# Kernel tuning notes

Measured on AMD Instinct MI355X. Metric: run time of the kernel, lower is better.

The kernel has to match this reference:

```python
import jax, jax.numpy as jnp
import numpy as np

B, S, IN_DIM, P_DIM, H = 2, 2048, 1024, 512, 8
HD = P_DIM // H
N_PENTA = 1024
SCALES = (128, 256, 512)
K_NEIGH = max(16, min(int(S * 0.15), 128))  # adaptive window -> 128
SCALE = 1.0 / float(np.sqrt(HD))
EPS = 1e-5


def _ln(x, g, b):
    mu = jnp.mean(x, axis=-1, keepdims=True)
    var = jnp.mean((x - mu) ** 2, axis=-1, keepdims=True)
    return (x - mu) * jax.lax.rsqrt(var + EPS) * g + b


def setup_inputs() -> dict:
    key = jax.random.key(0)
    ks = list(jax.random.split(key, 6 + 2 * len(SCALES)))
    w = lambda k, shp: jax.random.normal(k, shp, jnp.float32) * 0.02
    inp = {
        'sequence_features': jax.random.normal(ks[0], (B, S, IN_DIM), jnp.float32),
        'shared_pentachora': jax.random.normal(ks[1], (N_PENTA, 5, P_DIM), jnp.float32),
        'shared_positions': jax.random.uniform(ks[2], (N_PENTA,), dtype=jnp.float32),
        'proj_W': w(ks[3], (IN_DIM, P_DIM)), 'proj_b': jnp.zeros((P_DIM,), jnp.float32),
        'ln_g': jnp.ones((P_DIM,), jnp.float32), 'ln_b': jnp.zeros((P_DIM,), jnp.float32),
        'qkv_W': w(ks[4], (P_DIM, 3 * P_DIM)), 'qkv_b': jnp.zeros((3 * P_DIM,), jnp.float32),
        'out_W': w(ks[5], (P_DIM, P_DIM)), 'out_b': jnp.zeros((P_DIM,), jnp.float32),
    }
    i = 6
    for s in SCALES:
        inp[f'w1_{s}'] = w(ks[i], (P_DIM, 2 * s)); inp[f'b1_{s}'] = jnp.zeros((2 * s,), jnp.float32)
        inp[f'g_{s}'] = jnp.ones((2 * s,), jnp.float32); inp[f'bb_{s}'] = jnp.zeros((2 * s,), jnp.float32)
        inp[f'w2_{s}'] = w(ks[i + 1], (2 * s, s)); inp[f'b2_{s}'] = jnp.zeros((s,), jnp.float32)
        i += 2
    return inp


def _attend_one(z_b, pos_b, qkv_W, qkv_b, out_W, out_b):
    # z_b: [S, P_DIM], pos_b: [S]
    qkv = (z_b @ qkv_W + qkv_b).reshape(S, 3, H, HD)
    q = jnp.transpose(qkv[:, 0], (1, 0, 2))  # [H, S, HD]
    k = jnp.transpose(qkv[:, 1], (1, 0, 2))
    v = jnp.transpose(qkv[:, 2], (1, 0, 2))
    dist = jnp.abs(pos_b[:, None] - pos_b[None, :])  # [S, S]
    _, routes = jax.lax.top_k(-dist, K_NEIGH)        # [S, K] nearest in Cantor space
    kg = k[:, routes, :]  # [H, S, K, HD] gathered keys
    vg = v[:, routes, :]
    scores = jnp.einsum('hqd,hqkd->hqk', q, kg) * SCALE
    attn = jax.nn.softmax(scores, axis=-1)
    out = jnp.einsum('hqk,hqkd->hqd', attn, vg)
    out = jnp.transpose(out, (1, 0, 2)).reshape(S, P_DIM)
    return out @ out_W + out_b


def reference(sequence_features, shared_pentachora, shared_positions, proj_W, proj_b, ln_g, ln_b, qkv_W, qkv_b, out_W, out_b, w1_128, b1_128, g_128, bb_128, w2_128, b2_128, w1_256, b1_256, g_256, bb_256, w2_256, b2_256, w1_512, b1_512, g_512, bb_512, w2_512, b2_512):
    # centroids from pentachora vertices, L2-normalized
    cent = shared_pentachora.mean(axis=1)
    cent = cent / jnp.clip(jnp.linalg.norm(cent, axis=-1, keepdims=True), 1e-12)
    # input projection -> LN -> GELU -> L2 normalize
    z = jax.nn.gelu(_ln(sequence_features @ proj_W + proj_b, ln_g, ln_b), approximate=False)
    z = z / jnp.clip(jnp.linalg.norm(z, axis=-1, keepdims=True), 1e-12)
    # match to opinion anchors, inherit Cantor positions
    anchor_ids = jnp.argmax(jnp.einsum('bnd,pd->bnp', z, cent), axis=-1)  # [B, S]
    cantor_positions = shared_positions[anchor_ids]  # [B, S]
    # per-sample geometric sparse attention (vmapped over batch)
    z_att = jax.vmap(_attend_one, in_axes=(0, 0, None, None, None, None))(
        z, cantor_positions, qkv_W, qkv_b, out_W, out_b)  # [B, S, P_DIM]
    pooled = z_att.mean(axis=1)  # [B, P_DIM] (no attention mask)
    scale_params = (
        (w1_128, b1_128, g_128, bb_128, w2_128, b2_128),
        (w1_256, b1_256, g_256, bb_256, w2_256, b2_256),
        (w1_512, b1_512, g_512, bb_512, w2_512, b2_512),
    )
    outs = []
    for (w1, b1, g, bb, w2, b2) in scale_params:
        h = jax.nn.gelu(_ln(pooled @ w1 + b1, g, bb), approximate=False)
        outs.append(h @ w2 + b2)
    return jnp.concatenate(outs, axis=-1)  # [B, 128+256+512] concatenated scale opinions
```

## Files before the change

kernel.cpp:

```cpp
#include <hip/hip_runtime.h>
#include <math.h>

#define DEV __device__ __forceinline__

static constexpr int S_LEN  = 2048;
static constexpr int IN_DIM = 1024;
static constexpr int P_DIM  = 512;
static constexpr int NHEAD  = 8;
static constexpr int HD     = 64;
static constexpr int KN     = 128;

typedef __attribute__((ext_vector_type(8))) short bf16x8;
typedef __attribute__((ext_vector_type(4))) float f32x4;

DEV float gelu_exact(float x) {
    return 0.5f * x * (1.0f + erff(x * 0.70710678118654752440f));
}

DEV short bf_hi(float x) {
    unsigned u = __float_as_uint(x);
    unsigned r = (u + 0x7fffu + ((u >> 16) & 1u)) >> 16;
    return (short)r;
}
DEV float bf_f(short h) { return __uint_as_float(((unsigned)(unsigned short)h) << 16); }

DEV float block_reduce_sum(float v, float* sm4) {
    #pragma unroll
    for (int off = 32; off; off >>= 1) v += __shfl_down(v, off, 64);
    int lane = threadIdx.x & 63, w = threadIdx.x >> 6;
    __syncthreads();
    if (lane == 0) sm4[w] = v;
    __syncthreads();
    return sm4[0] + sm4[1] + sm4[2] + sm4[3];
}

DEV void wt_body(const float* __restrict__ W, short* __restrict__ WTh,
                 short* __restrict__ WTl, int K, int N, int bk, int bn,
                 float (*tile)[65]) {
    int t = threadIdx.x;
    int c = t & 63, r4 = t >> 6;
    #pragma unroll
    for (int i = 0; i < 16; i++) {
        int row = r4 + i * 4;
        tile[row][c] = W[(long)(bk * 64 + row) * N + bn * 64 + c];
    }
    __syncthreads();
    #pragma unroll
    for (int i = 0; i < 16; i++) {
        int n = r4 + i * 4;
        float v = tile[c][n];
        short h = bf_hi(v);
        long o = (long)(bn * 64 + n) * K + bk * 64 + c;
        WTh[o] = h;
        WTl[o] = bf_hi(v - bf_f(h));
    }
}

__global__ __launch_bounds__(256) void k_prep(const float* __restrict__ penta,
                                              short* __restrict__ ch, short* __restrict__ cl,
                                              const float* __restrict__ projW,
                                              short* __restrict__ pjh, short* __restrict__ pjl,
                                              const float* __restrict__ qkvW,
                                              short* __restrict__ qkh, short* __restrict__ qkl,
                                              const float* __restrict__ seq,
                                              short* __restrict__ sh, short* __restrict__ sl,
                                              unsigned long long* __restrict__ rowkey,
                                              float* __restrict__ pooledZ) {
    __shared__ float tile[64][65];
    __shared__ float sm4[4];
    int blk = blockIdx.x, t = threadIdx.x;
    if (blk < 1024) {
        int p = blk;
        if (t < 4) rowkey[p * 4 + t] = 0ull;
        if (p < 4) pooledZ[p * 256 + t] = 0.f;
        float c0 = 0.f, c1 = 0.f;
        #pragma unroll
        for (int v = 0; v < 5; v++) {
            const float* row = penta + ((long)p * 5 + v) * P_DIM;
            c0 += row[t];
            c1 += row[t + 256];
        }
        c0 /= 5.0f; c1 /= 5.0f;
        float tot = block_reduce_sum(c0 * c0 + c1 * c1, sm4);
        float n = fmaxf(sqrtf(tot), 1e-12f);
        float v0 = c0 / n, v1 = c1 / n;
        short h0 = bf_hi(v0), h1 = bf_hi(v1);
        ch[p * P_DIM + t]       = h0;
        ch[p * P_DIM + t + 256] = h1;
        cl[p * P_DIM + t]       = bf_hi(v0 - bf_f(h0));
        cl[p * P_DIM + t + 256] = bf_hi(v1 - bf_f(h1));
    } else if (blk < 1152) {
        int id = blk - 1024;
        wt_body(projW, pjh, pjl, IN_DIM, P_DIM, id & 15, id >> 4, tile);
    } else if (blk < 1344) {
        int id = blk - 1152;
        wt_body(qkvW, qkh, qkl, P_DIM, 3 * P_DIM, id & 7, id >> 3, tile);
    } else {
        long base = ((long)(blk - 1344) * 256 + t) * 16;
        #pragma unroll
        for (int u = 0; u < 4; u++) {
            float4 v = *(const float4*)(seq + base + u * 4);
            short h0 = bf_hi(v.x), h1 = bf_hi(v.y), h2 = bf_hi(v.z), h3 = bf_hi(v.w);
            *(short4*)(sh + base + u * 4) = make_short4(h0, h1, h2, h3);
            *(short4*)(sl + base + u * 4) =
                make_short4(bf_hi(v.x - bf_f(h0)), bf_hi(v.y - bf_f(h1)),
                            bf_hi(v.z - bf_f(h2)), bf_hi(v.w - bf_f(h3)));
        }
    }
}

template <int BM, int K, int N, int EPI>
__global__ __launch_bounds__(256) void k_mm(const short* __restrict__ Ash,
                                            const short* __restrict__ Asl,
                                            const short* __restrict__ BTh,
                                            const short* __restrict__ BTl,
                                            const float* __restrict__ bias,
                                            float* __restrict__ C,
                                            unsigned long long* __restrict__ rowkey) {
    constexpr int TI  = BM / 32;
    constexpr int CA  = BM / 8;
    constexpr int NCH = 2 * CA + 32;
    __shared__ __align__(128) short AhS[BM * 64], AlS[BM * 64];
    __shared__ __align__(128) short BhS[128 * 64], BlS[128 * 64];
    int t = threadIdx.x;
    int lane = t & 63, wave = t >> 6;
    int wr = (wave >> 1) * (BM / 2), wc = (wave & 1) * 64;
    int m = lane & 15, quad = lane >> 4;
    int rb = blockIdx.x * BM, cb = blockIdx.y * 128;
    int r8 = lane >> 3, p8 = lane & 7;
    int sl = p8 ^ r8;

    f32x4 acc[TI][4];
    #pragma unroll
    for (int i = 0; i < TI; i++)
        #pragma unroll
        for (int j = 0; j < 4; j++) acc[i][j] = (f32x4){0.f, 0.f, 0.f, 0.f};

    for (int k0 = 0; k0 < K; k0 += 64) {
        __syncthreads();
        for (int c = wave; c < NCH; c += 4) {
            const short* src; short* dst;
            if (c < CA) {
                src = Ash + (long)(rb + c * 8 + r8) * K + k0 + sl * 8;
                dst = AhS + c * 512;
            } else if (c < 2 * CA) {
                int cc = c - CA;
                src = Asl + (long)(rb + cc * 8 + r8) * K + k0 + sl * 8;
                dst = AlS + cc * 512;
            } else if (c < 2 * CA + 16) {
                int cc = c - 2 * CA;
                src = BTh + (long)(cb + cc * 8 + r8) * K + k0 + sl * 8;
                dst = BhS + cc * 512;
            } else {
                int cc = c - 2 * CA - 16;
                src = BTl + (long)(cb + cc * 8 + r8) * K + k0 + sl * 8;
                dst = BlS + cc * 512;
            }
            __builtin_amdgcn_global_load_lds(
                (const __attribute__((address_space(1))) unsigned int*)src,
                (__attribute__((address_space(3))) unsigned int*)dst, 16, 0, 0);
        }
        __syncthreads();

        #pragma unroll
        for (int ks = 0; ks < 2; ks++) {
            int so = ((ks * 4 + quad) ^ (m & 7)) * 8;
            bf16x8 ah[TI], al[TI], bh[4], bl[4];
            #pragma unroll
            for (int i = 0; i < TI; i++) {
                int off = (wr + i * 16 + m) * 64 + so;
                ah[i] = *(const bf16x8*)(AhS + off);
                al[i] = *(const bf16x8*)(AlS + off);
            }
            #pragma unroll
            for (int j = 0; j < 4; j++) {
                int off = (wc + j * 16 + m) * 64 + so;
                bh[j] = *(const bf16x8*)(BhS + off);
                bl[j] = *(const bf16x8*)(BlS + off);
            }
            #pragma unroll
            for (int i = 0; i < TI; i++)
                #pragma unroll
                for (int j = 0; j < 4; j++) {
                    acc[i][j] = __builtin_amdgcn_mfma_f32_16x16x32_bf16(ah[i], bh[j], acc[i][j], 0, 0, 0);
                    acc[i][j] = __builtin_amdgcn_mfma_f32_16x16x32_bf16(ah[i], bl[j], acc[i][j], 0, 0, 0);
                    acc[i][j] = __builtin_amdgcn_mfma_f32_16x16x32_bf16(al[i], bh[j], acc[i][j], 0, 0, 0);
                }
        }
    }

    if (EPI == 0) {
        #pragma unroll
        for (int i = 0; i < TI; i++) {
            int gr0 = rb + wr + i * 16 + quad * 4;
            #pragma unroll
            for (int j = 0; j < 4; j++) {
                int gc = cb + wc + j * 16 + m;
                float bv = bias[gc];
                #pragma unroll
                for (int r = 0; r < 4; r++)
                    C[(long)(gr0 + r) * N + gc] = acc[i][j][r] + bv;
            }
        }
    } else {
        #pragma unroll
        for (int i = 0; i < TI; i++) {
            #pragma unroll
            for (int r = 0; r < 4; r++) {
                int gr = rb + wr + i * 16 + quad * 4 + r;
                float bv = acc[i][0][r];
                int bp = cb + wc + m;
                #pragma unroll
                for (int j = 1; j < 4; j++) {
                    float v = acc[i][j][r];
                    int p = cb + wc + j * 16 + m;
                    if (v > bv) { bv = v; bp = p; }
                }
                #pragma unroll
                for (int off = 1; off < 16; off <<= 1) {
                    float ov = __shfl_xor(bv, off, 64);
                    int op = __shfl_xor(bp, off, 64);
                    if (ov > bv || (ov == bv && op < bp)) { bv = ov; bp = op; }
                }
                if (m == 0) {
                    unsigned u = __float_as_uint(bv);
                    u = (u & 0x80000000u) ? ~u : (u | 0x80000000u);
                    unsigned long long key =
                        ((unsigned long long)u << 32) | (unsigned)(0xFFFFFFFFu - (unsigned)bp);
                    atomicMax(&rowkey[gr], key);
                }
            }
        }
    }
}

__global__ __launch_bounds__(256) void k_ln_gelu_norm(const float* __restrict__ Zin,
                                                      const float* __restrict__ g,
                                                      const float* __restrict__ b,
                                                      short* __restrict__ z_h,
                                                      short* __restrict__ z_l) {
    long row = blockIdx.x;
    int t = threadIdx.x;
    __shared__ float sm4[4];
    float x0 = Zin[row * P_DIM + t], x1 = Zin[row * P_DIM + t + 256];
    float mu = block_reduce_sum(x0 + x1, sm4) * (1.0f / P_DIM);
    float d0 = x0 - mu, d1 = x1 - mu;
    float var = block_reduce_sum(d0 * d0 + d1 * d1, sm4) * (1.0f / P_DIM);
    float rs = 1.0f / sqrtf(var + 1e-5f);
    float y0 = gelu_exact(d0 * rs * g[t] + b[t]);
    float y1 = gelu_exact(d1 * rs * g[t + 256] + b[t + 256]);
    float nn = block_reduce_sum(y0 * y0 + y1 * y1, sm4);
    float n = fmaxf(sqrtf(nn), 1e-12f);
    float v0 = y0 / n, v1 = y1 / n;
    short h0 = bf_hi(v0), h1 = bf_hi(v1);
    z_h[row * P_DIM + t]       = h0;
    z_h[row * P_DIM + t + 256] = h1;
    z_l[row * P_DIM + t]       = bf_hi(v0 - bf_f(h0));
    z_l[row * P_DIM + t + 256] = bf_hi(v1 - bf_f(h1));
}

__global__ __launch_bounds__(256) void k_rank(const unsigned long long* __restrict__ rowkey,
                                              const float* __restrict__ spos,
                                              int* __restrict__ order,
                                              float* __restrict__ pos_srt) {
    int b = blockIdx.y, t = threadIdx.x;
    __shared__ unsigned long long key[2048];
    for (int u = 0; u < 8; u++) {
        int i = t + u * 256;
        unsigned p = 0xFFFFFFFFu - (unsigned)(rowkey[b * 2048 + i] & 0xFFFFFFFFull);
        key[i] = (((unsigned long long)__float_as_uint(spos[p])) << 32) | (unsigned)i;
    }
    __syncthreads();
    int i = blockIdx.x * 256 + t;
    unsigned long long ki = key[i];
    int rank = 0;
    #pragma unroll 8
    for (int j = 0; j < 2048; j++) rank += (key[j] < ki) ? 1 : 0;
    order[b * 2048 + rank]   = i;
    pos_srt[b * 2048 + rank] = __uint_as_float((unsigned)(ki >> 32));
}

__global__ __launch_bounds__(256) void k_routes(const float* __restrict__ pos_srt,
                                                const int* __restrict__ order,
                                                unsigned long long* __restrict__ bmG,
                                                uint2* __restrict__ bounds) {
    int blk = blockIdx.x;
    int b = blk >> 9;
    int t = threadIdx.x;
    int lane = t & 63, wave = t >> 6;
    int r = (blk & 511) * 4 + wave;
    __shared__ float ps[2048];
    __shared__ unsigned short tk[2048];
    for (int u = 0; u < 8; u++) {
        int i = t + u * 256;
        ps[i] = pos_srt[b * 2048 + i];
        tk[i] = (unsigned short)order[b * 2048 + i];
    }
    __syncthreads();

    float pi = ps[r];
    float T = 3e38f;
    #pragma unroll
    for (int a2 = 0; a2 < 2; a2++) {
        int a = lane + a2 * 64;
        int jl = r - a, jr = r + 127 - a;
        if (jl >= 0 && jr <= 2047) {
            float dl = (a > 0)   ? (pi - ps[jl]) : 0.f;
            float dr = (a < 127) ? (ps[jr] - pi) : 0.f;
            T = fminf(T, fmaxf(dl, dr));
        }
    }
    #pragma unroll
    for (int off = 1; off < 64; off <<= 1) T = fminf(T, __shfl_xor(T, off, 64));

    int lo = 0, hi = r;
    while (lo < hi) { int mid = (lo + hi) >> 1; if (pi - ps[mid] <= T) hi = mid; else lo = mid + 1; }
    int mn = lo;
    lo = r; hi = 2047;
    while (lo < hi) { int mid = (lo + hi + 1) >> 1; if (ps[mid] - pi <= T) lo = mid; else hi = mid - 1; }
    int mx = lo;
    int Ls, Rs;
    if (T > 0.f) {
        lo = 0; hi = r;
        while (lo < hi) { int mid = (lo + hi) >> 1; if (pi - ps[mid] < T) hi = mid; else lo = mid + 1; }
        Ls = lo;
        lo = r; hi = 2047;
        while (lo < hi) { int mid = (lo + hi + 1) >> 1; if (ps[mid] - pi < T) lo = mid; else hi = mid - 1; }
        Rs = lo;
    } else { Ls = r + 1; Rs = r - 1; }

    int cnt_strict = (Rs >= Ls) ? (Rs - Ls + 1) : 0;
    int need = 128 - cnt_strict;
    int l0a, l0b, r0a, r0b;
    if (cnt_strict > 0) { l0a = mn; l0b = Ls - 1; r0a = Rs + 1; r0b = mx; }
    else                { l0a = mn; l0b = mx;     r0a = 1;      r0b = 0; }
    int nL = (l0b >= l0a) ? (l0b - l0a + 1) : 0;
    int nR = (r0b >= r0a) ? (r0b - r0a + 1) : 0;
    int tiecount = nL + nR;

    int X = 65535;
    if (need < tiecount) {
        int lo2 = 0, hi2 = 2047;
        while (lo2 < hi2) {
            int mid = (lo2 + hi2) >> 1;
            int cnt = 0;
            for (int e = lane; e < tiecount; e += 64) {
                int j = (e < nL) ? (l0a + e) : (r0a + e - nL);
                cnt += (tk[j] <= mid) ? 1 : 0;
            }
            #pragma unroll
            for (int off = 1; off < 64; off <<= 1) cnt += __shfl_xor(cnt, off, 64);
            if (cnt >= need) hi2 = mid; else lo2 = mid + 1;
        }
        X = lo2;
    }

    int qlo_loc = 1 << 30, qhi_loc = -1;
    if (lane < 32) {
        unsigned long long bits = 0;
        int j0 = lane << 6, j1 = j0 + 63;
        if (cnt_strict > 0) {
            int a0 = max(Ls, j0), a1 = min(Rs, j1);
            if (a0 <= a1) {
                int s = a0 - j0, e = a1 - j0;
                unsigned long long msk = (e - s == 63) ? ~0ull
                                       : (((1ull << (e - s + 1)) - 1) << s);
                bits |= msk;
            }
        }
        int a0 = max(l0a, j0), a1 = min(l0b, j1);
        for (int j = a0; j <= a1; j++) if (tk[j] <= X) bits |= 1ull << (j - j0);
        a0 = max(r0a, j0); a1 = min(r0b, j1);
        for (int j = a0; j <= a1; j++) if (tk[j] <= X) bits |= 1ull << (j - j0);
        if (bits) {
            qlo_loc = j0 + __builtin_ctzll(bits);
            qhi_loc = j0 + 63 - __builtin_clzll(bits);
        }
        bmG[((long)(b * 2048 + r)) * 32 + lane] = bits;
    }
    #pragma unroll
    for (int off = 1; off < 64; off <<= 1) {
        qlo_loc = min(qlo_loc, __shfl_xor(qlo_loc, off, 64));
        qhi_loc = max(qhi_loc, __shfl_xor(qhi_loc, off, 64));
    }
    if (lane == 0)
        bounds[b * 2048 + r] = make_uint2((unsigned)qlo_loc, (unsigned)qhi_loc);
}

__global__ __launch_bounds__(256) void k_kv(const float* __restrict__ qkv,
                                            const int* __restrict__ order,
                                            short* __restrict__ Ks_h,
                                            short* __restrict__ Ks_l,
                                            short* __restrict__ Vt_h) {
    __shared__ short tile[64][72];
    int blk = blockIdx.x, t = threadIdx.x;
    if (blk < 512) {
        int b = blk >> 8, bx = blk & 255;
        int lr = t >> 5;
        int seg = t & 31;
        int rank = bx * 8 + lr;
        int tok = order[b * 2048 + rank];
        const float4* src = (const float4*)qkv + (long)(b * 2048 + tok) * 384 + 128 + seg * 4;
        long dsto = (long)(b * 2048 + rank) * 512 + seg * 16;
        #pragma unroll
        for (int u = 0; u < 4; u++) {
            float4 v = src[u];
            short h0 = bf_hi(v.x), h1 = bf_hi(v.y), h2 = bf_hi(v.z), h3 = bf_hi(v.w);
            *(short4*)(Ks_h + dsto + u * 4) = make_short4(h0, h1, h2, h3);
            *(short4*)(Ks_l + dsto + u * 4) =
                make_short4(bf_hi(v.x - bf_f(h0)), bf_hi(v.y - bf_f(h1)),
                            bf_hi(v.z - bf_f(h2)), bf_hi(v.w - bf_f(h3)));
        }
    } else {
        int id = blk - 512;
        int rt = id & 31, dt = (id >> 5) & 7, b = id >> 8;
        int lr = t >> 2;
        int q4 = t & 3;
        int tok = order[b * 2048 + rt * 64 + lr];
        const float4* src = (const float4*)qkv + (long)(b * 2048 + tok) * 384 + 256 + dt * 16;
        #pragma unroll
        for (int u = 0; u < 4; u++) {
            float4 v = src[q4 + u * 4];
            int d0 = (q4 + u * 4) * 4;
            tile[d0 + 0][lr] = bf_hi(v.x);
            tile[d0 + 1][lr] = bf_hi(v.y);
            tile[d0 + 2][lr] = bf_hi(v.z);
            tile[d0 + 3][lr] = bf_hi(v.w);
        }
        __syncthreads();
        int d = t >> 2, c4 = t & 3;
        long o = ((long)(b * 512 + dt * 64 + d)) * 2048 + rt * 64 + c4 * 16;
        #pragma unroll
        for (int j = 0; j < 4; j++)
            *(short4*)(Vt_h + o + j * 4) = make_short4(tile[d][c4 * 16 + j * 4 + 0],
                                                       tile[d][c4 * 16 + j * 4 + 1],
                                                       tile[d][c4 * 16 + j * 4 + 2],
                                                       tile[d][c4 * 16 + j * 4 + 3]);
    }
}

__global__ __launch_bounds__(256) void k_attn(const float* __restrict__ qkv,
                                              const int* __restrict__ order,
                                              const unsigned long long* __restrict__ bmG,
                                              const uint2* __restrict__ bounds,
                                              const short* __restrict__ Ks_h,
                                              const short* __restrict__ Ks_l,
                                              const short* __restrict__ Vt_h,
                                              float* __restrict__ pooledZ) {
    __shared__ __align__(16) char smem[17280];
    short* Pt = (short*)smem;
    unsigned short* cm = (unsigned short*)(smem + 10240);
    float* Opart = (float*)smem;
    float2* ml = (float2*)(smem + 16384);
    int* sh_tok = (int*)(smem + 16896);
    int* sh_lohi = (int*)(smem + 16960);
    float2* sc = (float2*)(smem + 16968);

    int gb = blockIdx.x;
    int b  = gb >> 9;
    int qg = (gb >> 2) & 127;
    int hp = gb & 3;
    int h0 = hp * 2;
    int r0 = qg * 16;
    int t = threadIdx.x;
    int lane = t & 63, wave = t >> 6;
    int rh = wave & 1, hs = wave >> 1;
    int key = lane & 15, quad = lane >> 4;

    const float4* qkvF4 = (const float4*)qkv;

    if (t < 16) sh_tok[t] = order[b * 2048 + r0 + t];
    if (t == 0) { sh_lohi[0] = 1 << 30; sh_lohi[1] = 0; }
    #pragma unroll
    for (int u = 0; u < 8; u++) {
        int e = t + u * 256;
        int c = e >> 4, q = e & 15;
        cm[c * 16 + q] = (unsigned short)(
            (bmG[((long)(b * 2048 + r0 + q)) * 32 + (c >> 2)] >> ((c & 3) * 16)) & 0xFFFF);
    }
    __syncthreads();
    if (t < 16) {
        uint2 bd = bounds[b * 2048 + r0 + t];
        atomicMin(&sh_lohi[0], (int)bd.x);
        atomicMax(&sh_lohi[1], (int)bd.y);
    }

    bf16x8 qh[2], ql[2];
    {
        long tq = (long)(b * 2048 + sh_tok[key]) * 384;
        #pragma unroll
        for (int ks = 0; ks < 2; ks++) {
            float4 v0 = qkvF4[tq + (h0 + hs) * 16 + ks * 8 + quad * 2];
            float4 v1 = qkvF4[tq + (h0 + hs) * 16 + ks * 8 + quad * 2 + 1];
            float vv[8] = {v0.x, v0.y, v0.z, v0.w, v1.x, v1.y, v1.z, v1.w};
            #pragma unroll
            for (int j = 0; j < 8; j++) {
                short hb = bf_hi(vv[j]);
                qh[ks][j] = hb;
                ql[ks][j] = bf_hi(vv[j] - bf_f(hb));
            }
        }
    }
    __syncthreads();
    int lo = sh_lohi[0] & ~63, hi = sh_lohi[1] + 1;

    float mrow[4], lrow[4];
    f32x4 Ont[4];
    #pragma unroll
    for (int r = 0; r < 4; r++) { mrow[r] = -1e30f; lrow[r] = 0.f; }
    #pragma unroll
    for (int nt = 0; nt < 4; nt++) Ont[nt] = (f32x4){0.f, 0.f, 0.f, 0.f};

    short* PtH = Pt + wave * 1280;
    short* PtL = PtH + 640;

    int hd = h0 + hs;
    long kbase = ((long)b * 2048) * 512 + hd * 64 + quad * 8;
    long vbase = ((long)(b * 512 + hd * 64 + key)) * 2048;

    for (int c0 = lo; c0 < hi; c0 += 64) {
        int cb = c0 + rh * 32;
        if (cb >= hi) continue;
        int ch0 = cb >> 4;
        unsigned long long m0 = *(const unsigned long long*)(cm + ch0 * 16 + quad * 4);
        unsigned long long m1 = (ch0 + 1 < 128)
            ? *(const unsigned long long*)(cm + (ch0 + 1) * 16 + quad * 4) : 0ull;
        if (!__any((m0 | m1) != 0ull)) continue;

        long kr0 = kbase + (long)(cb + key) * 512;
        long kr1 = kbase + (long)(cb + 16 + key) * 512;

        f32x4 S0 = (f32x4){0.f,0.f,0.f,0.f}, S1 = (f32x4){0.f,0.f,0.f,0.f};
        #pragma unroll
        for (int ks = 0; ks < 2; ks++) {
            bf16x8 b0h = *(const bf16x8*)(Ks_h + kr0 + ks * 32);
            bf16x8 b0l = *(const bf16x8*)(Ks_l + kr0 + ks * 32);
            bf16x8 b1h = *(const bf16x8*)(Ks_h + kr1 + ks * 32);
            bf16x8 b1l = *(const bf16x8*)(Ks_l + kr1 + ks * 32);
            S0 = __builtin_amdgcn_mfma_f32_16x16x32_bf16(qh[ks], b0h, S0, 0, 0, 0);
            S0 = __builtin_amdgcn_mfma_f32_16x16x32_bf16(qh[ks], b0l, S0, 0, 0, 0);
            S0 = __builtin_amdgcn_mfma_f32_16x16x32_bf16(ql[ks], b0h, S0, 0, 0, 0);
            S1 = __builtin_amdgcn_mfma_f32_16x16x32_bf16(qh[ks], b1h, S1, 0, 0, 0);
            S1 = __builtin_amdgcn_mfma_f32_16x16x32_bf16(qh[ks], b1l, S1, 0, 0, 0);
            S1 = __builtin_amdgcn_mfma_f32_16x16x32_bf16(ql[ks], b1h, S1, 0, 0, 0);
        }
        float s0[4], s1[4], p0[4], p1[4];
        unsigned bit0[4], bit1[4];
        #pragma unroll
        for (int r = 0; r < 4; r++) {
            bit0[r] = (unsigned)((m0 >> (r * 16 + key)) & 1);
            bit1[r] = (unsigned)((m1 >> (r * 16 + key)) & 1);
            s0[r] = bit0[r] ? S0[r] * 0.125f : -1e30f;
            s1[r] = bit1[r] ? S1[r] * 0.125f : -1e30f;
        }
        #pragma unroll
        for (int r = 0; r < 4; r++) {
            float cmax = fmaxf(s0[r], s1[r]);
            cmax = fmaxf(cmax, __shfl_xor(cmax, 1, 64));
            cmax = fmaxf(cmax, __shfl_xor(cmax, 2, 64));
            cmax = fmaxf(cmax, __shfl_xor(cmax, 4, 64));
            cmax = fmaxf(cmax, __shfl_xor(cmax, 8, 64));
            float mn = fmaxf(mrow[r], cmax);
            float alpha = __expf(mrow[r] - mn);
            mrow[r] = mn;
            p0[r] = bit0[r] ? __expf(s0[r] - mn) : 0.f;
            p1[r] = bit1[r] ? __expf(s1[r] - mn) : 0.f;
            float rs = p0[r] + p1[r];
            rs += __shfl_xor(rs, 1, 64);
            rs += __shfl_xor(rs, 2, 64);
            rs += __shfl_xor(rs, 4, 64);
            rs += __shfl_xor(rs, 8, 64);
            lrow[r] = lrow[r] * alpha + rs;
            #pragma unroll
            for (int nt = 0; nt < 4; nt++) Ont[nt][r] *= alpha;
        }
        #pragma unroll
        for (int r = 0; r < 4; r++) {
            short ha = bf_hi(p0[r]);
            PtH[(quad * 4 + r) * 40 + key] = ha;
            PtL[(quad * 4 + r) * 40 + key] = bf_hi(p0[r] - bf_f(ha));
            short hb = bf_hi(p1[r]);
            PtH[(quad * 4 + r) * 40 + 16 + key] = hb;
            PtL[(quad * 4 + r) * 40 + 16 + key] = bf_hi(p1[r] - bf_f(hb));
        }
        bf16x8 pfh = *(const bf16x8*)(PtH + key * 40 + quad * 8);
        bf16x8 pfl = *(const bf16x8*)(PtL + key * 40 + quad * 8);
        #pragma unroll
        for (int nt = 0; nt < 4; nt++) {
            bf16x8 vf = *(const bf16x8*)(Vt_h + vbase + (long)nt * 16 * 2048
                                         + cb + quad * 8);
            Ont[nt] = __builtin_amdgcn_mfma_f32_16x16x32_bf16(pfh, vf, Ont[nt], 0, 0, 0);
            Ont[nt] = __builtin_amdgcn_mfma_f32_16x16x32_bf16(pfl, vf, Ont[nt], 0, 0, 0);
        }
    }

    if (key == 0) {
        #pragma unroll
        for (int r = 0; r < 4; r++)
            ml[(rh * 2 + hs) * 16 + quad * 4 + r] = make_float2(mrow[r], lrow[r]);
    }
    __syncthreads();
    #pragma unroll
    for (int nt = 0; nt < 4; nt++)
        #pragma unroll
        for (int r = 0; r < 4; r++)
            Opart[rh * 2048 + (quad * 4 + r) * 128 + hs * 64 + nt * 16 + key] = Ont[nt][r];

    if (t < 32) {
        int q = t >> 1, hs2 = t & 1;
        float2 a = ml[(0 * 2 + hs2) * 16 + q];
        float2 c = ml[(1 * 2 + hs2) * 16 + q];
        float M = fmaxf(a.x, c.x);
        float w0 = __expf(a.x - M), w1 = __expf(c.x - M);
        float inv = 1.0f / fmaxf(a.y * w0 + c.y * w1, 1e-37f);
        sc[hs2 * 16 + q] = make_float2(w0 * inv, w1 * inv);
    }
    __syncthreads();

    if (t < 128) {
        int d = t, hs2 = d >> 6;
        float s = 0.f;
        #pragma unroll
        for (int q = 0; q < 16; q++) {
            float2 w = sc[hs2 * 16 + q];
            s += Opart[q * 128 + d] * w.x + Opart[2048 + q * 128 + d] * w.y;
        }
        atomicAdd(&pooledZ[b * P_DIM + h0 * HD + d], s);
    }
}

__global__ __launch_bounds__(256) void k_opool(const float* __restrict__ pooledZ,
                                               const float* __restrict__ outW,
                                               const float* __restrict__ outb,
                                               float* __restrict__ pooled) {
    int b = blockIdx.y, t = threadIdx.x;
    int c = blockIdx.x * 256 + t;
    __shared__ float pz[P_DIM];
    pz[t]       = pooledZ[b * P_DIM + t];
    pz[t + 256] = pooledZ[b * P_DIM + t + 256];
    __syncthreads();
    float acc = 0.f;
    #pragma unroll 8
    for (int d = 0; d < P_DIM; d++) acc = fmaf(pz[d], outW[d * P_DIM + c], acc);
    pooled[b * P_DIM + c] = acc + (float)S_LEN * outb[c];
}

__global__ __launch_bounds__(256) void k_exp_fc1(const float* __restrict__ pooled,
                                                 const float* __restrict__ w1_0, const float* __restrict__ b1_0,
                                                 const float* __restrict__ w1_1, const float* __restrict__ b1_1,
                                                 const float* __restrict__ w1_2, const float* __restrict__ b1_2,
                                                 float* __restrict__ h) {
    int t = threadIdx.x, b = blockIdx.y;
    int c = blockIdx.x * 256 + t;
    __shared__ float pl[P_DIM];
    pl[t]       = pooled[b * P_DIM + t]       * (1.0f / S_LEN);
    pl[t + 256] = pooled[b * P_DIM + t + 256] * (1.0f / S_LEN);
    __syncthreads();

    const float* wp; const float* bp; int s2, j;
    if (c < 256)      { wp = w1_0; bp = b1_0; s2 = 256;  j = c; }
    else if (c < 768) { wp = w1_1; bp = b1_1; s2 = 512;  j = c - 256; }
    else              { wp = w1_2; bp = b1_2; s2 = 1024; j = c - 768; }

    const float* p = wp + j;
    float acc = 0.f;
    #pragma unroll 16
    for (int k = 0; k < P_DIM; k++) {
        acc = fmaf(pl[k], *p, acc);
        p += s2;
    }
    h[(long)b * 1792 + c] = acc + bp[j];
}

__global__ __launch_bounds__(256) void k_exp_ln(float* __restrict__ h,
                                                const float* __restrict__ g0, const float* __restrict__ bb0,
                                                const float* __restrict__ g1, const float* __restrict__ bb1,
                                                const float* __restrict__ g2, const float* __restrict__ bb2) {
    int e = blockIdx.x, b = blockIdx.y, t = threadIdx.x;
    __shared__ float sm4[4];
    const int offs[3] = {0, 256, 768};
    const int ns[3]   = {256, 512, 1024};
    const float* gs[3]  = {g0, g1, g2};
    const float* bbs[3] = {bb0, bb1, bb2};
    int n = ns[e];
    float* hp = h + (long)b * 1792 + offs[e];
    const float* g = gs[e]; const float* bb = bbs[e];

    float x[4];
    float loc = 0.f;
    for (int u = 0; u < 4; u++) {
        int j = t + u * 256;
        x[u] = (j < n) ? hp[j] : 0.f;
        loc += x[u];
    }
    float mu = block_reduce_sum(loc, sm4) / (float)n;
    loc = 0.f;
    for (int u = 0; u < 4; u++) {
        int j = t + u * 256;
        if (j < n) { float d = x[u] - mu; loc += d * d; }
    }
    float var = block_reduce_sum(loc, sm4) / (float)n;
    float rs = 1.0f / sqrtf(var + 1e-5f);
    for (int u = 0; u < 4; u++) {
        int j = t + u * 256;
        if (j < n) hp[j] = gelu_exact((x[u] - mu) * rs * g[j] + bb[j]);
    }
}

__global__ __launch_bounds__(256) void k_exp_fc2(const float* __restrict__ h,
                                                 const float* __restrict__ w2_0, const float* __restrict__ b2_0,
                                                 const float* __restrict__ w2_1, const float* __restrict__ b2_1,
                                                 const float* __restrict__ w2_2, const float* __restrict__ b2_2,
                                                 float* __restrict__ out) {
    int t = threadIdx.x, b = blockIdx.y;
    int c = blockIdx.x * 256 + t;
    __shared__ float hs[1792];
    for (int u = 0; u < 7; u++) hs[t + u * 256] = h[(long)b * 1792 + t + u * 256];
    __syncthreads();
    if (c >= 896) return;

    const float* wp; const float* bp; int s2, sN, j, off_h;
    if (c < 128)      { wp = w2_0; bp = b2_0; s2 = 256;  sN = 128; j = c;       off_h = 0; }
    else if (c < 384) { wp = w2_1; bp = b2_1; s2 = 512;  sN = 256; j = c - 128; off_h = 256; }
    else              { wp = w2_2; bp = b2_2; s2 = 1024; sN = 512; j = c - 384; off_h = 768; }

    const float* p = wp + j;
    const float* hh = hs + off_h;
    float acc = 0.f;
    #pragma unroll 16
    for (int k = 0; k < s2; k++) {
        acc = fmaf(hh[k], *p, acc);
        p += sN;
    }
    out[b * 896 + c] = acc + bp[j];
}

extern "C" void kernel_launch(void* const* d_in, const int* in_sizes, int n_in,
                              void* d_out, int out_size, void* d_ws, size_t ws_size,
                              hipStream_t stream) {
    const float* seq   = (const float*)d_in[0];
    const float* penta = (const float*)d_in[1];
    const float* spos  = (const float*)d_in[2];
    const float* projW = (const float*)d_in[3];
    const float* projb = (const float*)d_in[4];
    const float* lng   = (const float*)d_in[5];
    const float* lnb   = (const float*)d_in[6];
    const float* qkvW  = (const float*)d_in[7];
    const float* qkvb  = (const float*)d_in[8];
    const float* outW  = (const float*)d_in[9];
    const float* outb  = (const float*)d_in[10];

    float* ws      = (float*)d_ws;
    float* z_pre   = ws;
    short* z_h     = (short*)(z_pre + 2097152);
    short* z_l     = z_h + 2097152;
    float* qkv     = (float*)(z_l + 2097152);
    float* pooledZ = qkv + 6291456;
    float* pooled  = pooledZ + 4096;
    float* hbuf    = pooled + 1024;
    unsigned long long* rowkey = (unsigned long long*)(hbuf + 4096);
    float* pos_srt = (float*)(rowkey + 4096);
    int*   order   = (int*)(pos_srt + 4096);
    uint2* bounds  = (uint2*)(order + 4096);
    unsigned long long* bmG = (unsigned long long*)(bounds + 4096);
    short* cent_h  = (short*)(bmG + 131072);
    short* cent_l  = cent_h + 524288;
    short* pjWT_h  = cent_l + 524288;
    short* pjWT_l  = pjWT_h + 524288;
    short* qkWT_h  = pjWT_l + 524288;
    short* qkWT_l  = qkWT_h + 786432;

    short* seq_h = (short*)qkv;
    short* seq_l = seq_h + 4194304;
    short* Ks_h = (short*)z_pre;
    short* Ks_l = Ks_h + 2097152;
    short* Vt_h = cent_h;

    k_prep<<<2368, 256, 0, stream>>>(penta, cent_h, cent_l,
                                     projW, pjWT_h, pjWT_l,
                                     qkvW, qkWT_h, qkWT_l,
                                     seq, seq_h, seq_l,
                                     rowkey, pooledZ);

    { dim3 g(64, 4);  k_mm<64, IN_DIM, P_DIM, 0><<<g, 256, 0, stream>>>(
          seq_h, seq_l, pjWT_h, pjWT_l, projb, z_pre, nullptr); }
    k_ln_gelu_norm<<<4096, 256, 0, stream>>>(z_pre, lng, lnb, z_h, z_l);

    { dim3 g(32, 8);  k_mm<128, P_DIM, 1024, 1><<<g, 256, 0, stream>>>(
          z_h, z_l, cent_h, cent_l, nullptr, nullptr, rowkey); }
    { dim3 g(8, 2);   k_rank<<<g, 256, 0, stream>>>(rowkey, spos, order, pos_srt); }

    { dim3 g(32, 12); k_mm<128, P_DIM, 3 * P_DIM, 0><<<g, 256, 0, stream>>>(
          z_h, z_l, qkWT_h, qkWT_l, qkvb, qkv, nullptr); }
    k_routes<<<1024, 256, 0, stream>>>(pos_srt, order, bmG, bounds);
    k_kv<<<1024, 256, 0, stream>>>(qkv, order, Ks_h, Ks_l, Vt_h);
    k_attn<<<1024, 256, 0, stream>>>(qkv, order, bmG, bounds,
                                     Ks_h, Ks_l, Vt_h, pooledZ);

    { dim3 g(2, 2); k_opool<<<g, 256, 0, stream>>>(pooledZ, outW, outb, pooled); }
    { dim3 g1(7, 2);
      k_exp_fc1<<<g1, 256, 0, stream>>>(pooled,
        (const float*)d_in[11], (const float*)d_in[12],
        (const float*)d_in[17], (const float*)d_in[18],
        (const float*)d_in[23], (const float*)d_in[24], hbuf); }
    { dim3 g2(3, 2);
      k_exp_ln<<<g2, 256, 0, stream>>>(hbuf,
        (const float*)d_in[13], (const float*)d_in[14],
        (const float*)d_in[19], (const float*)d_in[20],
        (const float*)d_in[25], (const float*)d_in[26]); }
    { dim3 g3(4, 2);
      k_exp_fc2<<<g3, 256, 0, stream>>>(hbuf,
        (const float*)d_in[15], (const float*)d_in[16],
        (const float*)d_in[21], (const float*)d_in[22],
        (const float*)d_in[27], (const float*)d_in[28], (float*)d_out); }
}
```

Measured before the change: 397.3 us.

## Pre-transpose tail weights and use wave-per-output GEMVs for pooled MLP

The out-projection and the three expert FC1/FC2 weight matrices are now transposed once into workspace inside the prep kernel. The tail GEMVs each assign one wavefront per output column and reduce with shuffles, replacing the old scheme of a few blocks where each thread walked a whole strided column. The aim is to spread these tiny serial GEMVs across many more CUs with coalesced weight reads. The cost is extra prep blocks and extra workspace traffic for the transposes.

```diff
diff --git a/kernel.cpp b/kernel.cpp
--- a/kernel.cpp
+++ b/kernel.cpp
@@ -32,6 +32,12 @@
     if (lane == 0) sm4[w] = v;
     __syncthreads();
     return sm4[0] + sm4[1] + sm4[2] + sm4[3];
+}
+
+DEV float wave_sum(float v) {
+    #pragma unroll
+    for (int off = 32; off; off >>= 1) v += __shfl_xor(v, off, 64);
+    return v;
 }
 
 DEV void wt_body(const float* __restrict__ W, short* __restrict__ WTh,
@@ -53,6 +59,23 @@
         long o = (long)(bn * 64 + n) * K + bk * 64 + c;
         WTh[o] = h;
         WTl[o] = bf_hi(v - bf_f(h));
+    }
+}
+
+DEV void t32_body(const float* __restrict__ W, float* __restrict__ WT,
+                  int K, int N, int bk, int bn, float (*tile)[65]) {
+    int t = threadIdx.x;
+    int c = t & 63, r4 = t >> 6;
+    #pragma unroll
+    for (int i = 0; i < 16; i++) {
+        int row = r4 + i * 4;
+        tile[row][c] = W[(long)(bk * 64 + row) * N + bn * 64 + c];
+    }
+    __syncthreads();
+    #pragma unroll
+    for (int i = 0; i < 16; i++) {
+        int n = r4 + i * 4;
+        WT[(long)(bn * 64 + n) * K + bk * 64 + c] = tile[c][n];
     }
 }
 
@@ -65,7 +88,14 @@
                                               const float* __restrict__ seq,
                                               short* __restrict__ sh, short* __restrict__ sl,
                                               unsigned long long* __restrict__ rowkey,
-                                              float* __restrict__ pooledZ) {
+                                              float* __restrict__ pooledZ,
+                                              const float* __restrict__ outW, float* __restrict__ outWT,
+                                              const float* __restrict__ w1_0,
+                                              const float* __restrict__ w1_1,
+                                              const float* __restrict__ w1_2, float* __restrict__ w1T,
+                                              const float* __restrict__ w2_0,
+                                              const float* __restrict__ w2_1,
+                                              const float* __restrict__ w2_2, float* __restrict__ w2T) {
     __shared__ float tile[64][65];
     __shared__ float sm4[4];
     int blk = blockIdx.x, t = threadIdx.x;
@@ -95,7 +125,7 @@
     } else if (blk < 1344) {
         int id = blk - 1152;
         wt_body(qkvW, qkh, qkl, P_DIM, 3 * P_DIM, id & 7, id >> 3, tile);
-    } else {
+    } else if (blk < 2368) {
         long base = ((long)(blk - 1344) * 256 + t) * 16;
         #pragma unroll
         for (int u = 0; u < 4; u++) {
@@ -106,6 +136,27 @@
                 make_short4(bf_hi(v.x - bf_f(h0)), bf_hi(v.y - bf_f(h1)),
                             bf_hi(v.z - bf_f(h2)), bf_hi(v.w - bf_f(h3)));
         }
+    } else if (blk < 2432) {
+        int id = blk - 2368;
+        t32_body(outW, outWT, 512, 512, id & 7, id >> 3, tile);
+    } else if (blk < 2464) {
+        int id = blk - 2432;
+        t32_body(w1_0, w1T, 512, 256, id & 7, id >> 3, tile);
+    } else if (blk < 2528) {
+        int id = blk - 2464;
+        t32_body(w1_1, w1T + 256 * 512, 512, 512, id & 7, id >> 3, tile);
+    } else if (blk < 2656) {
+        int id = blk - 2528;
+        t32_body(w1_2, w1T + 768 * 512, 512, 1024, id & 7, id >> 3, tile);
+    } else if (blk < 2664) {
+        int id = blk - 2656;
+        t32_body(w2_0, w2T, 256, 128, id & 3, id >> 2, tile);
+    } else if (blk < 2696) {
+        int id = blk - 2664;
+        t32_body(w2_1, w2T + 32768, 512, 256, id & 7, id >> 3, tile);
+    } else {
+        int id = blk - 2696;
+        t32_body(w2_2, w2T + 163840, 1024, 512, id & 15, id >> 4, tile);
     }
 }
 
@@ -629,47 +680,69 @@
     }
 }
 
-__global__ __launch_bounds__(256) void k_opool(const float* __restrict__ pooledZ,
-                                               const float* __restrict__ outW,
-                                               const float* __restrict__ outb,
-                                               float* __restrict__ pooled) {
+__global__ __launch_bounds__(256) void k_gemv_opool(const float* __restrict__ pooledZ,
+                                                    const float* __restrict__ outWT,
+                                                    const float* __restrict__ outb,
+                                                    float* __restrict__ pooled) {
     int b = blockIdx.y, t = threadIdx.x;
-    int c = blockIdx.x * 256 + t;
+    int lane = t & 63, w = t >> 6;
     __shared__ float pz[P_DIM];
     pz[t]       = pooledZ[b * P_DIM + t];
     pz[t + 256] = pooledZ[b * P_DIM + t + 256];
     __syncthreads();
+    int c = blockIdx.x * 4 + w;
+    const float* wp = outWT + (long)c * 512;
     float acc = 0.f;
-    #pragma unroll 8
-    for (int d = 0; d < P_DIM; d++) acc = fmaf(pz[d], outW[d * P_DIM + c], acc);
-    pooled[b * P_DIM + c] = acc + (float)S_LEN * outb[c];
-}
-
-__global__ __launch_bounds__(256) void k_exp_fc1(const float* __restrict__ pooled,
-                                                 const float* __restrict__ w1_0, const float* __restrict__ b1_0,
-                                                 const float* __restrict__ w1_1, const float* __restrict__ b1_1,
-                                                 const float* __restrict__ w1_2, const float* __restrict__ b1_2,
-                                                 float* __restrict__ h) {
-    int t = threadIdx.x, b = blockIdx.y;
-    int c = blockIdx.x * 256 + t;
+    #pragma unroll
+    for (int i = 0; i < 8; i++) acc = fmaf(pz[lane + i * 64], wp[lane + i * 64], acc);
+    acc = wave_sum(acc);
+    if (lane == 0) pooled[b * P_DIM + c] = acc + (float)S_LEN * outb[c];
+}
+
+__global__ __launch_bounds__(256) void k_gemv_fc1(const float* __restrict__ pooled,
+                                                  const float* __restrict__ w1T,
+                                                  const float* __restrict__ b1_0,
+                                                  const float* __restrict__ b1_1,
+                                                  const float* __restrict__ b1_2,
+                                                  float* __restrict__ h) {
+    int b = blockIdx.y, t = threadIdx.x;
+    int lane = t & 63, w = t >> 6;
     __shared__ float pl[P_DIM];
     pl[t]       = pooled[b * P_DIM + t]       * (1.0f / S_LEN);
     pl[t + 256] = pooled[b * P_DIM + t + 256] * (1.0f / S_LEN);
     __syncthreads();
-
-    const float* wp; const float* bp; int s2, j;
-    if (c < 256)      { wp = w1_0; bp = b1_0; s2 = 256;  j = c; }
-    else if (c < 768) { wp = w1_1; bp = b1_1; s2 = 512;  j = c - 256; }
-    else              { wp = w1_2; bp = b1_2; s2 = 1024; j = c - 768; }
-
-    const float* p = wp + j;
+    int c = blockIdx.x * 4 + w;
+    const float* wp = w1T + (long)c * 512;
     float acc = 0.f;
-    #pragma unroll 16
-    for (int k = 0; k < P_DIM; k++) {
-        acc = fmaf(pl[k], *p, acc);
-        p += s2;
-    }
-    h[(long)b * 1792 + c] = acc + bp[j];
+    #pragma unroll
+    for (int i = 0; i < 8; i++) acc = fmaf(pl[lane + i * 64], wp[lane + i * 64], acc);
+    acc = wave_sum(acc);
+    if (lane == 0) {
+        float bb = (c < 256) ? b1_0[c] : (c < 768) ? b1_1[c - 256] : b1_2[c - 768];
+        h[(long)b * 1792 + c] = acc + bb;
+    }
+}
+
+__global__ __launch_bounds__(256) void k_gemv_fc2(const float* __restrict__ h,
+                                                  const float* __restrict__ w2T,
+                                                  const float* __restrict__ b2_0,
+                                                  const float* __restrict__ b2_1,
+                                                  const float* __restrict__ b2_2,
+                                                  float* __restrict__ out) {
+    int b = blockIdx.y, t = threadIdx.x;
+    int lane = t & 63, w = t >> 6;
+    __shared__ float hh[1792];
+    for (int u = 0; u < 7; u++) hh[t + u * 256] = h[(long)b * 1792 + t + u * 256];
+    __syncthreads();
+    int c = blockIdx.x * 4 + w;
+    const float* wp; const float* hp; int s2; float bb;
+    if (c < 128)      { wp = w2T + (long)c * 256;                hp = hh;       s2 = 256;  bb = b2_0[c]; }
+    else if (c < 384) { wp = w2T + 32768 + (long)(c - 128) * 512;  hp = hh + 256; s2 = 512;  bb = b2_1[c - 128]; }
+    else              { wp = w2T + 163840 + (long)(c - 384) * 1024; hp = hh + 768; s2 = 1024; bb = b2_2[c - 384]; }
+    float acc = 0.f;
+    for (int i = lane; i < s2; i += 64) acc = fmaf(hp[i], wp[i], acc);
+    acc = wave_sum(acc);
+    if (lane == 0) out[b * 896 + c] = acc + bb;
 }
 
 __global__ __launch_bounds__(256) void k_exp_ln(float* __restrict__ h,
@@ -705,34 +778,6 @@
         int j = t + u * 256;
         if (j < n) hp[j] = gelu_exact((x[u] - mu) * rs * g[j] + bb[j]);
     }
-}
-
-__global__ __launch_bounds__(256) void k_exp_fc2(const float* __restrict__ h,
-                                                 const float* __restrict__ w2_0, const float* __restrict__ b2_0,
-                                                 const float* __restrict__ w2_1, const float* __restrict__ b2_1,
-                                                 const float* __restrict__ w2_2, const float* __restrict__ b2_2,
-                                                 float* __restrict__ out) {
-    int t = threadIdx.x, b = blockIdx.y;
-    int c = blockIdx.x * 256 + t;
-    __shared__ float hs[1792];
-    for (int u = 0; u < 7; u++) hs[t + u * 256] = h[(long)b * 1792 + t + u * 256];
-    __syncthreads();
-    if (c >= 896) return;
-
-    const float* wp; const float* bp; int s2, sN, j, off_h;
-    if (c < 128)      { wp = w2_0; bp = b2_0; s2 = 256;  sN = 128; j = c;       off_h = 0; }
-    else if (c < 384) { wp = w2_1; bp = b2_1; s2 = 512;  sN = 256; j = c - 128; off_h = 256; }
-    else              { wp = w2_2; bp = b2_2; s2 = 1024; sN = 512; j = c - 384; off_h = 768; }
-
-    const float* p = wp + j;
-    const float* hh = hs + off_h;
-    float acc = 0.f;
-    #pragma unroll 16
-    for (int k = 0; k < s2; k++) {
-        acc = fmaf(hh[k], *p, acc);
-        p += sN;
-    }
-    out[b * 896 + c] = acc + bp[j];
 }
 
 extern "C" void kernel_launch(void* const* d_in, const int* in_sizes, int n_in,
@@ -769,6 +814,9 @@
     short* pjWT_l  = pjWT_h + 524288;
     short* qkWT_h  = pjWT_l + 524288;
     short* qkWT_l  = qkWT_h + 786432;
+    float* outWT   = (float*)(qkWT_l + 786432);
+    float* w1T     = outWT + 262144;
+    float* w2T     = w1T + 917504;
 
     short* seq_h = (short*)qkv;
     short* seq_l = seq_h + 4194304;
@@ -776,11 +824,18 @@
     short* Ks_l = Ks_h + 2097152;
     short* Vt_h = cent_h;
 
-    k_prep<<<2368, 256, 0, stream>>>(penta, cent_h, cent_l,
+    k_prep<<<2824, 256, 0, stream>>>(penta, cent_h, cent_l,
                                      projW, pjWT_h, pjWT_l,
                                      qkvW, qkWT_h, qkWT_l,
                                      seq, seq_h, seq_l,
-                                     rowkey, pooledZ);
+                                     rowkey, pooledZ,
+                                     outW, outWT,
+                                     (const float*)d_in[11],
+                                     (const float*)d_in[17],
+                                     (const float*)d_in[23], w1T,
+                                     (const float*)d_in[15],
+                                     (const float*)d_in[21],
+                                     (const float*)d_in[27], w2T);
 
     { dim3 g(64, 4);  k_mm<64, IN_DIM, P_DIM, 0><<<g, 256, 0, stream>>>(
           seq_h, seq_l, pjWT_h, pjWT_l, projb, z_pre, nullptr); }
@@ -797,20 +852,14 @@
     k_attn<<<1024, 256, 0, stream>>>(qkv, order, bmG, bounds,
                                      Ks_h, Ks_l, Vt_h, pooledZ);
 
-    { dim3 g(2, 2); k_opool<<<g, 256, 0, stream>>>(pooledZ, outW, outb, pooled); }
-    { dim3 g1(7, 2);
-      k_exp_fc1<<<g1, 256, 0, stream>>>(pooled,
-        (const float*)d_in[11], (const float*)d_in[12],
-        (const float*)d_in[17], (const float*)d_in[18],
-        (const float*)d_in[23], (const float*)d_in[24], hbuf); }
-    { dim3 g2(3, 2);
-      k_exp_ln<<<g2, 256, 0, stream>>>(hbuf,
+    { dim3 g(128, 2); k_gemv_opool<<<g, 256, 0, stream>>>(pooledZ, outWT, outb, pooled); }
+    { dim3 g(448, 2); k_gemv_fc1<<<g, 256, 0, stream>>>(pooled, w1T,
+        (const float*)d_in[12], (const float*)d_in[18], (const float*)d_in[24], hbuf); }
+    { dim3 g(3, 2);   k_exp_ln<<<g, 256, 0, stream>>>(hbuf,
         (const float*)d_in[13], (const float*)d_in[14],
         (const float*)d_in[19], (const float*)d_in[20],
         (const float*)d_in[25], (const float*)d_in[26]); }
-    { dim3 g3(4, 2);
-      k_exp_fc2<<<g3, 256, 0, stream>>>(hbuf,
-        (const float*)d_in[15], (const float*)d_in[16],
-        (const float*)d_in[21], (const float*)d_in[22],
-        (const float*)d_in[27], (const float*)d_in[28], (float*)d_out); }
-}
+    { dim3 g(224, 2); k_gemv_fc2<<<g, 256, 0, stream>>>(hbuf, w2T,
+        (const float*)d_in[16], (const float*)d_in[22], (const float*)d_in[28],
+        (float*)d_out); }
+}
```

Result: faster. 332.6 us (-16.3%).
